# Kernel tuning notes

Hardware: AMD Instinct MI355X
Metric: run time of the kernel (lower is better)

The kernel has to match this reference:

```python
import jax, jax.numpy as jnp
import numpy as np

B, T, C = 4, 2048, 1024
T_REF = 512
H = 16
D = C // H


def setup_inputs() -> dict:
    key = jax.random.key(0)
    ks = jax.random.split(key, 16)
    s = 0.02
    return {
        "x": jax.random.normal(ks[0], (B, T, C), jnp.float32),
        "ref_feat": jax.random.normal(ks[1], (B, T_REF, C), jnp.float32),
        "Wq": jax.random.normal(ks[2], (C, C), jnp.float32) * s,
        "bq": jax.random.normal(ks[3], (C,), jnp.float32) * s,
        "Wk": jax.random.normal(ks[4], (C, C), jnp.float32) * s,
        "bk": jax.random.normal(ks[5], (C,), jnp.float32) * s,
        "Wv": jax.random.normal(ks[6], (C, C), jnp.float32) * s,
        "bv": jax.random.normal(ks[7], (C,), jnp.float32) * s,
        "Wrk": jax.random.normal(ks[8], (C, C), jnp.float32) * s,
        "brk": jax.random.normal(ks[9], (C,), jnp.float32) * s,
        "Wrv": jax.random.normal(ks[10], (C, C), jnp.float32) * s,
        "brv": jax.random.normal(ks[11], (C,), jnp.float32) * s,
        "Wp": jax.random.normal(ks[12], (C, C), jnp.float32) * s,
        "bp": jax.random.normal(ks[13], (C,), jnp.float32) * s,
    }


def _heads(y):
    # [B, T, C] -> [B, H, T, D]
    b, t, c = y.shape
    return y.reshape(b, t, H, D).transpose(0, 2, 1, 3)


def reference(x, ref_feat, Wq, bq, Wk, bk, Wv, bv, Wrk, brk, Wrv, brv, Wp, bp):
    b, t, c = x.shape
    t_ref = ref_feat.shape[1]
    q = _heads(x @ Wq + bq)                      # [B,H,T,D]
    k = _heads(x @ Wk + bk)                      # [B,H,T,D]
    v = _heads(x @ Wv + bv)
    ref_k = _heads(ref_feat @ Wrk + brk)         # [B,H,Tref,D]
    ref_v = _heads(ref_feat @ Wrv + brv)
    k = jnp.concatenate([k, ref_k], axis=2)      # [B,H,T+Tref,D]
    v = jnp.concatenate([v, ref_v], axis=2)

    # additive bias: causal over self keys, fully visible over ref keys
    causal = jnp.tril(jnp.ones((t, t), dtype=bool))
    full_mask = jnp.concatenate([causal, jnp.ones((t, t_ref), dtype=bool)], axis=1)
    bias = jnp.where(full_mask, 0.0, -jnp.inf).astype(x.dtype)  # [T, T+Tref]

    scale = 1.0 / jnp.sqrt(jnp.asarray(D, x.dtype))
    scores = jnp.einsum("bhtd,bhsd->bhts", q, k) * scale + bias
    attn = jax.nn.softmax(scores, axis=-1)
    y = jnp.einsum("bhts,bhsd->bhtd", attn, v)   # [B,H,T,D]
    y = y.transpose(0, 2, 1, 3).reshape(b, t, c)
    return y @ Wp + bp
```

## Files before the change

### kernel.cpp

```cpp
#include <hip/hip_runtime.h>
#include <hip/hip_bf16.h>

typedef short s16x4 __attribute__((ext_vector_type(4)));
typedef short s16x8 __attribute__((ext_vector_type(8)));
typedef __bf16 bf16x8 __attribute__((ext_vector_type(8)));
typedef float f32x4 __attribute__((ext_vector_type(4)));

#define DEVI static __device__ __forceinline__
#define QSCALE 0.18033688011112042f

DEVI unsigned short f2bf(float x) {
  union { float f; unsigned u; } a; a.f = x;
  unsigned r = a.u + 0x7fffu + ((a.u >> 16) & 1u);
  return (unsigned short)(r >> 16);
}
DEVI bf16x8 asbf(s16x8 v) {
  union { s16x8 s; bf16x8 b; } u; u.s = v; return u.b;
}
DEVI unsigned cvtpk(float lo, float hi) {
  unsigned r;
  asm("v_cvt_pk_bf16_f32 %0, %1, %2" : "=v"(r) : "v"(lo), "v"(hi));
  return r;
}
DEVI void gload16(const void* g, void* l) {
  __builtin_amdgcn_global_load_lds(
      (const __attribute__((address_space(1))) void*)g,
      (__attribute__((address_space(3))) void*)l, 16, 0, 0);
}

struct PrepArgs {
  const float* x; const float* ref; unsigned short* xg;
  const float* w[6]; unsigned short* o[6];
};

__global__ __launch_bounds__(256)
void prep(PrepArgs a) {
  __shared__ short tile[64][65];
  const int bid = blockIdx.x, t = threadIdx.x;
  if (bid < 5120) {
    int f = bid * 256 + t;
    int row = f >> 7, c8 = f & 127;
    const float* src = (row < 8192 ? a.x + (size_t)row * 1024
                                   : a.ref + (size_t)(row - 8192) * 1024) + c8 * 8;
    float4 v0 = *(const float4*)src;
    float4 v1 = *(const float4*)(src + 4);
    s16x8 o;
    o[0] = (short)f2bf(v0.x); o[1] = (short)f2bf(v0.y);
    o[2] = (short)f2bf(v0.z); o[3] = (short)f2bf(v0.w);
    o[4] = (short)f2bf(v1.x); o[5] = (short)f2bf(v1.y);
    o[6] = (short)f2bf(v1.z); o[7] = (short)f2bf(v1.w);
    int cs = (c8 & ~7) | ((c8 ^ row) & 7);
    *(s16x8*)(a.xg + (size_t)row * 1024 + cs * 8) = o;
  } else {
    int q = bid - 5120;
    int z = q >> 8, b2 = q & 255;
    const float* __restrict__ W = a.w[z];
    unsigned short* __restrict__ WT = a.o[z];
    const float sc = (z == 0) ? QSCALE : 1.0f;
    const int n0 = (b2 & 15) * 64;
    const int k0 = (b2 >> 4) * 64;
#pragma unroll
    for (int i = 0; i < 4; i++) {
      int f = t + i * 256;
      int r = f >> 4, c = (f & 15) * 4;
      float4 v = *(const float4*)(W + (size_t)(k0 + r) * 1024 + n0 + c);
      tile[r][c + 0] = (short)f2bf(v.x * sc);
      tile[r][c + 1] = (short)f2bf(v.y * sc);
      tile[r][c + 2] = (short)f2bf(v.z * sc);
      tile[r][c + 3] = (short)f2bf(v.w * sc);
    }
    __syncthreads();
#pragma unroll
    for (int i = 0; i < 2; i++) {
      int f = t + i * 256;
      int r = f >> 3, c8 = f & 7;
      s16x8 o;
#pragma unroll
      for (int jj = 0; jj < 8; jj++) o[jj] = tile[c8 * 8 + jj][r];
      *(s16x8*)(WT + (size_t)(n0 + r) * 1024 + k0 + ((c8 ^ (r & 7)) & 7) * 8) = o;
    }
  }
}

template<int MODE>
__global__ __launch_bounds__(256, 3)
void gemm_bt(const unsigned short* __restrict__ A, const unsigned short* __restrict__ BT,
             const float* __restrict__ b0, const float* __restrict__ b1,
             const float* __restrict__ b2,
             void* __restrict__ o0, void* __restrict__ o1, void* __restrict__ o2)
{
  const int K = 1024;
  __shared__ __align__(16) short As[128][64];
  __shared__ __align__(16) short Bs[128][64];
  const int t = threadIdx.x;
  const int lane = t & 63, wid = t >> 6;
  const int wm = wid >> 1, wn = wid & 1;
  const int lr = lane & 15, lg = lane >> 4;
  const size_t m0 = (size_t)blockIdx.y * 128;
  const int n0 = blockIdx.x * 128;

  f32x4 acc[4][4];
#pragma unroll
  for (int i = 0; i < 4; i++)
#pragma unroll
    for (int j = 0; j < 4; j++) acc[i][j] = (f32x4){0.f, 0.f, 0.f, 0.f};

  const unsigned short* Abase = A + m0 * K;
  const unsigned short* Bbase = BT + (size_t)n0 * K;
  const int r_ld = t >> 3, cb_ld = t & 7;

  for (int k0 = 0; k0 < K; k0 += 64) {
#pragma unroll
    for (int i = 0; i < 4; i++) {
      int r = r_ld + i * 32;
      gload16(Abase + (size_t)r * K + k0 + cb_ld * 8,
              (short*)As + (i * 256 + wid * 64) * 8);
      gload16(Bbase + (size_t)r * K + k0 + cb_ld * 8,
              (short*)Bs + (i * 256 + wid * 64) * 8);
    }
    __syncthreads();
#pragma unroll
    for (int ks = 0; ks < 2; ks++) {
      s16x8 af[4], bfr[4];
#pragma unroll
      for (int i = 0; i < 4; i++)
        af[i] = *(const s16x8*)&As[wm * 64 + i * 16 + lr][(((ks * 4 + lg) ^ lr) & 7) * 8];
#pragma unroll
      for (int i = 0; i < 4; i++)
        bfr[i] = *(const s16x8*)&Bs[wn * 64 + i * 16 + lr][(((ks * 4 + lg) ^ lr) & 7) * 8];
#pragma unroll
      for (int mi = 0; mi < 4; mi++)
#pragma unroll
        for (int ni = 0; ni < 4; ni++)
          acc[mi][ni] = __builtin_amdgcn_mfma_f32_16x16x32_bf16(
              asbf(af[mi]), asbf(bfr[ni]), acc[mi][ni], 0, 0, 0);
    }
    __syncthreads();
  }

  const int seg = n0 >> 10;
  const float* bb = (seg == 0) ? b0 : (seg == 1 ? b1 : b2);
#pragma unroll
  for (int mi = 0; mi < 4; mi++) {
#pragma unroll
    for (int ni = 0; ni < 4; ni++) {
      int cg = n0 + wn * 64 + ni * 16 + lr;
      int c = cg & 1023;
      float bv = bb[c];
      if (MODE == 0 && seg == 0) bv *= QSCALE;
      const bool vseg = (MODE == 0 && seg == 2) || (MODE == 1 && seg == 1);
      if (MODE != 2 && vseg) {
        int rm0 = (int)m0 + wm * 64 + mi * 16 + lg * 4;
        int d = c & 63, hh = c >> 6;
        int bb_, s;
        if (MODE == 0) { bb_ = rm0 >> 11; s = rm0 & 2047; }
        else           { bb_ = rm0 >> 9;  s = 2048 + (rm0 & 511); }
        int scol = (s & ~63) + ((((s >> 3) ^ d) & 7) << 3) + (s & 7);
        unsigned short* dst = (unsigned short*)(MODE == 0 ? o2 : o1);
        short4 pk4;
        pk4.x = (short)f2bf(acc[mi][ni][0] + bv);
        pk4.y = (short)f2bf(acc[mi][ni][1] + bv);
        pk4.z = (short)f2bf(acc[mi][ni][2] + bv);
        pk4.w = (short)f2bf(acc[mi][ni][3] + bv);
        *(short4*)(dst + ((size_t)(bb_ * 16 + hh) * 64 + d) * 2560 + scol) = pk4;
      } else {
#pragma unroll
        for (int r = 0; r < 4; r++) {
          int rm = (int)m0 + wm * 64 + mi * 16 + lg * 4 + r;
          float val = acc[mi][ni][r] + bv;
          if (MODE == 2) {
            ((float*)o0)[(size_t)rm * 1024 + cg] = val;
          } else {
            size_t orow; unsigned short* dst; bool swz;
            if (MODE == 0) {
              if (seg == 0) { dst = (unsigned short*)o0; orow = rm; swz = false; }
              else { orow = (size_t)(rm >> 11) * 2560 + (rm & 2047);
                     dst = (unsigned short*)o1; swz = true; }
            } else {
              orow = (size_t)(rm >> 9) * 2560 + 2048 + (rm & 511);
              dst = (unsigned short*)o0; swz = true;
            }
            int cc = c;
            if (swz) cc = (c & ~63) | ((((c >> 3) ^ (int)orow) & 7) << 3) | (c & 7);
            dst[orow * 1024 + cc] = f2bf(val);
          }
        }
      }
    }
  }
}

__global__ __launch_bounds__(256, 5)
void attn(const unsigned short* __restrict__ Q, const unsigned short* __restrict__ Kb,
          const unsigned short* __restrict__ VbT, unsigned short* __restrict__ Y)
{
  const int T = 2048, S = 2560, C = 1024, TREF = 512;
  __shared__ __align__(16) short Ks[2][64][64];
  __shared__ __align__(16) short Vt[2][64][64];
  const int t = threadIdx.x;
  const int lane = t & 63, wid = t >> 6;
  const int lr = lane & 15, lg = lane >> 4;

  const int bid = blockIdx.x;
  const int xcd = bid & 7, idx = bid >> 3;
  const int g = idx & 7;
  const int bx = 31 - (idx >> 3);
  const int bh = xcd * 8 + g;
  const int b = bh >> 4;
  const int hc = (bh & 15) * 64;
  const int q0 = bx * 64;

  const int nself = bx + 1;
  const int ntiles = nself + TREF / 64;

  auto s0_of = [&](int ti2) {
    return (ti2 < nself) ? ti2 * 64 : T + (ti2 - nself) * 64;
  };
  const int r_ld = t >> 3, cb_ld = t & 7;
  auto load_K = [&](int ti2, int buf) {
    int s0 = s0_of(ti2);
    const unsigned short* Krow = Kb + (size_t)(b * S + s0) * C + hc;
#pragma unroll
    for (int i = 0; i < 2; i++)
      gload16(Krow + (size_t)(r_ld + i * 32) * C + cb_ld * 8,
              (short*)&Ks[buf][0][0] + (i * 256 + wid * 64) * 8);
  };
  auto load_V = [&](int ti2, int buf) {
    int s0 = s0_of(ti2);
    const unsigned short* Vr = VbT + (size_t)bh * 64 * S + s0;
#pragma unroll
    for (int i = 0; i < 2; i++)
      gload16(Vr + (size_t)(r_ld + i * 32) * S + cb_ld * 8,
              (short*)&Vt[buf][0][0] + (i * 256 + wid * 64) * 8);
  };

  load_K(0, 0);
  load_V(0, 0);

  s16x8 qf[2];
  {
    size_t qrow = (size_t)(b * T + q0 + wid * 16 + lr);
#pragma unroll
    for (int ks = 0; ks < 2; ks++)
      qf[ks] = *(const s16x8*)(Q + qrow * C + hc + ks * 32 + lg * 8);
  }

  float mrow = -1e30f, lsum = 0.f;
  f32x4 o[4];
#pragma unroll
  for (int d = 0; d < 4; d++) o[d] = (f32x4){0.f, 0.f, 0.f, 0.f};

  __syncthreads();

  for (int ti = 0; ti < ntiles; ti++) {
    const int cur = ti & 1;
    const bool more = (ti + 1 < ntiles);
    if (more) { load_K(ti + 1, cur ^ 1); load_V(ti + 1, cur ^ 1); }

    f32x4 sa[4];
#pragma unroll
    for (int nt = 0; nt < 4; nt++) sa[nt] = (f32x4){0.f, 0.f, 0.f, 0.f};
    __builtin_amdgcn_s_setprio(1);
#pragma unroll
    for (int ks = 0; ks < 2; ks++) {
      s16x8 kf[4];
#pragma unroll
      for (int nt = 0; nt < 4; nt++)
        kf[nt] = *(const s16x8*)&Ks[cur][nt * 16 + lr][(((ks * 4 + lg) ^ lr) & 7) * 8];
#pragma unroll
      for (int nt = 0; nt < 4; nt++)
        sa[nt] = __builtin_amdgcn_mfma_f32_16x16x32_bf16(
            asbf(kf[nt]), asbf(qf[ks]), sa[nt], 0, 0, 0);
    }
    __builtin_amdgcn_s_setprio(0);

    if (ti == bx) {
      int qg = wid * 16 + lr;
#pragma unroll
      for (int nt = 0; nt < 4; nt++)
#pragma unroll
        for (int r = 0; r < 4; r++)
          if (nt * 16 + lg * 4 + r > qg) sa[nt][r] = -1e30f;
    }

    float mm[4];
#pragma unroll
    for (int nt = 0; nt < 4; nt++)
      mm[nt] = fmaxf(fmaxf(sa[nt][0], sa[nt][1]), fmaxf(sa[nt][2], sa[nt][3]));
    float lm = fmaxf(fmaxf(mm[0], mm[1]), fmaxf(mm[2], mm[3]));

    if (!__all(lm <= mrow + 8.f)) {
      float tm = lm;
      tm = fmaxf(tm, __shfl_xor(tm, 16, 64));
      tm = fmaxf(tm, __shfl_xor(tm, 32, 64));
      float mn = fmaxf(mrow, tm);
      float alpha = __builtin_amdgcn_exp2f(mrow - mn);
      mrow = mn;
      lsum *= alpha;
#pragma unroll
      for (int r = 0; r < 4; r++) {
        float ar = __shfl(alpha, lg * 4 + r, 64);
#pragma unroll
        for (int dt = 0; dt < 4; dt++) o[dt][r] *= ar;
      }
    }

    unsigned pk2[4][2];
    float rsn[4];
#pragma unroll
    for (int nt = 0; nt < 4; nt++) {
      float p0 = __builtin_amdgcn_exp2f(sa[nt][0] - mrow);
      float p1 = __builtin_amdgcn_exp2f(sa[nt][1] - mrow);
      float p2 = __builtin_amdgcn_exp2f(sa[nt][2] - mrow);
      float p3 = __builtin_amdgcn_exp2f(sa[nt][3] - mrow);
      rsn[nt] = (p0 + p1) + (p2 + p3);
      pk2[nt][0] = cvtpk(p0, p1);
      pk2[nt][1] = cvtpk(p2, p3);
    }
    lsum += (rsn[0] + rsn[1]) + (rsn[2] + rsn[3]);

    s16x8 pa[2];
#pragma unroll
    for (int ks = 0; ks < 2; ks++) {
      union { unsigned w[4]; s16x8 v; } U;
#pragma unroll
      for (int w = 0; w < 4; w++) {
        int srcL = lr + (((lg & 1) * 2 + (w >> 1)) << 4);
        unsigned v0 = __shfl((int)pk2[2 * ks][w & 1], srcL, 64);
        unsigned v1 = __shfl((int)pk2[2 * ks + 1][w & 1], srcL, 64);
        U.w[w] = (lg & 2) ? v1 : v0;
      }
      pa[ks] = U.v;
    }

    __builtin_amdgcn_s_setprio(1);
#pragma unroll
    for (int ks = 0; ks < 2; ks++) {
      s16x8 vf[4];
#pragma unroll
      for (int dt = 0; dt < 4; dt++)
        vf[dt] = *(const s16x8*)&Vt[cur][dt * 16 + lr][(((ks * 4 + lg) ^ lr) & 7) * 8];
#pragma unroll
      for (int dt = 0; dt < 4; dt++)
        o[dt] = __builtin_amdgcn_mfma_f32_16x16x32_bf16(
            asbf(pa[ks]), asbf(vf[dt]), o[dt], 0, 0, 0);
    }
    __builtin_amdgcn_s_setprio(0);

    __syncthreads();
  }

  float tot = lsum;
  tot += __shfl_xor(tot, 16, 64);
  tot += __shfl_xor(tot, 32, 64);
#pragma unroll
  for (int r = 0; r < 4; r++) {
    float inv = 1.0f / __shfl(tot, lg * 4 + r, 64);
    int qrow = b * T + q0 + wid * 16 + lg * 4 + r;
#pragma unroll
    for (int dt = 0; dt < 4; dt++) {
      int col = hc + dt * 16 + lr;
      int cb = col >> 3;
      int cs = (cb & ~7) | ((cb ^ qrow) & 7);
      Y[(size_t)qrow * C + cs * 8 + (col & 7)] = f2bf(o[dt][r] * inv);
    }
  }
}

extern "C" void kernel_launch(void* const* d_in, const int* in_sizes, int n_in,
                              void* d_out, int out_size, void* d_ws, size_t ws_size,
                              hipStream_t stream) {
  const float* x   = (const float*)d_in[0];
  const float* ref = (const float*)d_in[1];
  const float* Wq  = (const float*)d_in[2];
  const float* bq  = (const float*)d_in[3];
  const float* Wk  = (const float*)d_in[4];
  const float* bk  = (const float*)d_in[5];
  const float* Wv  = (const float*)d_in[6];
  const float* bv  = (const float*)d_in[7];
  const float* Wrk = (const float*)d_in[8];
  const float* brk = (const float*)d_in[9];
  const float* Wrv = (const float*)d_in[10];
  const float* brv = (const float*)d_in[11];
  const float* Wp  = (const float*)d_in[12];
  const float* bp  = (const float*)d_in[13];
  float* out = (float*)d_out;

  char* ws = (char*)d_ws;
  auto alloc = [&](size_t bytes) {
    char* p = ws; ws += (bytes + 255) & ~(size_t)255; return p;
  };
  const size_t WB = (size_t)1024 * 1024 * 2;
  unsigned short* Wall = (unsigned short*)alloc(5 * WB);
  unsigned short* WpT  = (unsigned short*)alloc(WB);
  unsigned short* xg  = (unsigned short*)alloc((size_t)10240 * 1024 * 2);
  unsigned short* rg  = xg + (size_t)8192 * 1024;
  unsigned short* qb  = (unsigned short*)alloc((size_t)8192 * 1024 * 2);
  unsigned short* kb  = (unsigned short*)alloc((size_t)4 * 2560 * 1024 * 2);
  unsigned short* vbT = (unsigned short*)alloc((size_t)4096 * 2560 * 2);
  unsigned short* yb  = (unsigned short*)alloc((size_t)8192 * 1024 * 2);

  dim3 tb(256);

  PrepArgs pa;
  pa.x = x; pa.ref = ref; pa.xg = xg;
  pa.w[0] = Wq;  pa.o[0] = Wall;
  pa.w[1] = Wk;  pa.o[1] = Wall + (size_t)1024 * 1024;
  pa.w[2] = Wv;  pa.o[2] = Wall + (size_t)2048 * 1024;
  pa.w[3] = Wrk; pa.o[3] = Wall + (size_t)3072 * 1024;
  pa.w[4] = Wrv; pa.o[4] = Wall + (size_t)4096 * 1024;
  pa.w[5] = Wp;  pa.o[5] = WpT;
  prep<<<dim3(6656), tb, 0, stream>>>(pa);

  gemm_bt<0><<<dim3(24, 64), tb, 0, stream>>>(xg, Wall, bq, bk, bv, qb, kb, vbT);
  gemm_bt<1><<<dim3(16, 16), tb, 0, stream>>>(rg, Wall + (size_t)3072 * 1024,
                                              brk, brv, nullptr, kb, vbT, nullptr);

  attn<<<dim3(2048), tb, 0, stream>>>(qb, kb, vbT, yb);

  gemm_bt<2><<<dim3(8, 64), tb, 0, stream>>>(yb, WpT, bp, bp, bp, out, out, out);
}
```

Before: 221.8 us.

## Pair causal query tiles per block and switch attention to 32x32 MFMA

Each attention block now handles two query tiles, bx and 31-bx, with two waves per tile, so every block does balanced causal work and shares the same streamed K/V tiles. The half-grid launch takes 1024 blocks instead of 2048. The inner products move from 16x16x32 to 32x32x16 bf16 MFMA, and P is repacked with permlane32 swaps instead of many shuffles. Output stores become 4-wide. This adds register pressure (launch bounds lowered to 4 waves per SIMD), and the low tile's waves idle on tiles past their diagonal.

```diff
diff --git a/kernel.cpp b/kernel.cpp
--- a/kernel.cpp
+++ b/kernel.cpp
@@ -5,6 +5,7 @@
 typedef short s16x8 __attribute__((ext_vector_type(8)));
 typedef __bf16 bf16x8 __attribute__((ext_vector_type(8)));
 typedef float f32x4 __attribute__((ext_vector_type(4)));
+typedef float f32x16 __attribute__((ext_vector_type(16)));
 
 #define DEVI static __device__ __forceinline__
 #define QSCALE 0.18033688011112042f
@@ -190,7 +191,7 @@
   }
 }
 
-__global__ __launch_bounds__(256, 5)
+__global__ __launch_bounds__(256, 4)
 void attn(const unsigned short* __restrict__ Q, const unsigned short* __restrict__ Kb,
           const unsigned short* __restrict__ VbT, unsigned short* __restrict__ Y)
 {
@@ -199,19 +200,20 @@
   __shared__ __align__(16) short Vt[2][64][64];
   const int t = threadIdx.x;
   const int lane = t & 63, wid = t >> 6;
-  const int lr = lane & 15, lg = lane >> 4;
+  const int l31 = lane & 31, hi = lane >> 5;
+  const int j = wid >> 1, sub = wid & 1;
 
   const int bid = blockIdx.x;
   const int xcd = bid & 7, idx = bid >> 3;
-  const int g = idx & 7;
-  const int bx = 31 - (idx >> 3);
-  const int bh = xcd * 8 + g;
+  const int bh = xcd * 8 + (idx >> 4);
+  const int bx = idx & 15;
   const int b = bh >> 4;
   const int hc = (bh & 15) * 64;
-  const int q0 = bx * 64;
-
-  const int nself = bx + 1;
+  const int qtile = j ? (31 - bx) : bx;
+
+  const int nself = 32 - bx;
   const int ntiles = nself + TREF / 64;
+  const int tdiag = j ? (nself - 1) : bx;
 
   auto s0_of = [&](int ti2) {
     return (ti2 < nself) ? ti2 * 64 : T + (ti2 - nself) * 64;
@@ -237,132 +239,144 @@
   load_K(0, 0);
   load_V(0, 0);
 
-  s16x8 qf[2];
+  s16x8 qf[4];
   {
-    size_t qrow = (size_t)(b * T + q0 + wid * 16 + lr);
-#pragma unroll
-    for (int ks = 0; ks < 2; ks++)
-      qf[ks] = *(const s16x8*)(Q + qrow * C + hc + ks * 32 + lg * 8);
+    size_t qrow = (size_t)(b * T + qtile * 64 + sub * 32 + l31);
+#pragma unroll
+    for (int ks = 0; ks < 4; ks++)
+      qf[ks] = *(const s16x8*)(Q + qrow * C + hc + ks * 16 + hi * 8);
   }
 
   float mrow = -1e30f, lsum = 0.f;
-  f32x4 o[4];
-#pragma unroll
-  for (int d = 0; d < 4; d++) o[d] = (f32x4){0.f, 0.f, 0.f, 0.f};
+  f32x16 o0 = 0.f, o1 = 0.f;
 
   __syncthreads();
+
+  const int swz = (l31 & 7);
 
   for (int ti = 0; ti < ntiles; ti++) {
     const int cur = ti & 1;
     const bool more = (ti + 1 < ntiles);
     if (more) { load_K(ti + 1, cur ^ 1); load_V(ti + 1, cur ^ 1); }
 
-    f32x4 sa[4];
-#pragma unroll
-    for (int nt = 0; nt < 4; nt++) sa[nt] = (f32x4){0.f, 0.f, 0.f, 0.f};
-    __builtin_amdgcn_s_setprio(1);
-#pragma unroll
-    for (int ks = 0; ks < 2; ks++) {
-      s16x8 kf[4];
-#pragma unroll
-      for (int nt = 0; nt < 4; nt++)
-        kf[nt] = *(const s16x8*)&Ks[cur][nt * 16 + lr][(((ks * 4 + lg) ^ lr) & 7) * 8];
-#pragma unroll
-      for (int nt = 0; nt < 4; nt++)
-        sa[nt] = __builtin_amdgcn_mfma_f32_16x16x32_bf16(
-            asbf(kf[nt]), asbf(qf[ks]), sa[nt], 0, 0, 0);
-    }
-    __builtin_amdgcn_s_setprio(0);
-
-    if (ti == bx) {
-      int qg = wid * 16 + lr;
-#pragma unroll
-      for (int nt = 0; nt < 4; nt++)
-#pragma unroll
-        for (int r = 0; r < 4; r++)
-          if (nt * 16 + lg * 4 + r > qg) sa[nt][r] = -1e30f;
-    }
-
-    float mm[4];
-#pragma unroll
-    for (int nt = 0; nt < 4; nt++)
-      mm[nt] = fmaxf(fmaxf(sa[nt][0], sa[nt][1]), fmaxf(sa[nt][2], sa[nt][3]));
-    float lm = fmaxf(fmaxf(mm[0], mm[1]), fmaxf(mm[2], mm[3]));
-
-    if (!__all(lm <= mrow + 8.f)) {
-      float tm = lm;
-      tm = fmaxf(tm, __shfl_xor(tm, 16, 64));
-      tm = fmaxf(tm, __shfl_xor(tm, 32, 64));
-      float mn = fmaxf(mrow, tm);
-      float alpha = __builtin_amdgcn_exp2f(mrow - mn);
-      mrow = mn;
-      lsum *= alpha;
-#pragma unroll
-      for (int r = 0; r < 4; r++) {
-        float ar = __shfl(alpha, lg * 4 + r, 64);
-#pragma unroll
-        for (int dt = 0; dt < 4; dt++) o[dt][r] *= ar;
-      }
-    }
-
-    unsigned pk2[4][2];
-    float rsn[4];
-#pragma unroll
-    for (int nt = 0; nt < 4; nt++) {
-      float p0 = __builtin_amdgcn_exp2f(sa[nt][0] - mrow);
-      float p1 = __builtin_amdgcn_exp2f(sa[nt][1] - mrow);
-      float p2 = __builtin_amdgcn_exp2f(sa[nt][2] - mrow);
-      float p3 = __builtin_amdgcn_exp2f(sa[nt][3] - mrow);
-      rsn[nt] = (p0 + p1) + (p2 + p3);
-      pk2[nt][0] = cvtpk(p0, p1);
-      pk2[nt][1] = cvtpk(p2, p3);
-    }
-    lsum += (rsn[0] + rsn[1]) + (rsn[2] + rsn[3]);
-
-    s16x8 pa[2];
-#pragma unroll
-    for (int ks = 0; ks < 2; ks++) {
-      union { unsigned w[4]; s16x8 v; } U;
-#pragma unroll
-      for (int w = 0; w < 4; w++) {
-        int srcL = lr + (((lg & 1) * 2 + (w >> 1)) << 4);
-        unsigned v0 = __shfl((int)pk2[2 * ks][w & 1], srcL, 64);
-        unsigned v1 = __shfl((int)pk2[2 * ks + 1][w & 1], srcL, 64);
-        U.w[w] = (lg & 2) ? v1 : v0;
-      }
-      pa[ks] = U.v;
-    }
-
-    __builtin_amdgcn_s_setprio(1);
-#pragma unroll
-    for (int ks = 0; ks < 2; ks++) {
-      s16x8 vf[4];
-#pragma unroll
-      for (int dt = 0; dt < 4; dt++)
-        vf[dt] = *(const s16x8*)&Vt[cur][dt * 16 + lr][(((ks * 4 + lg) ^ lr) & 7) * 8];
-#pragma unroll
-      for (int dt = 0; dt < 4; dt++)
-        o[dt] = __builtin_amdgcn_mfma_f32_16x16x32_bf16(
-            asbf(pa[ks]), asbf(vf[dt]), o[dt], 0, 0, 0);
-    }
-    __builtin_amdgcn_s_setprio(0);
+    const bool active = j || (ti <= bx) || (ti >= nself);
+    if (active) {
+      f32x16 sa0 = 0.f, sa1 = 0.f;
+      __builtin_amdgcn_s_setprio(1);
+#pragma unroll
+      for (int ks = 0; ks < 4; ks++) {
+        int cb = ks * 2 + hi;
+        s16x8 kf0 = *(const s16x8*)&Ks[cur][l31][((cb ^ swz) & 7) * 8];
+        s16x8 kf1 = *(const s16x8*)&Ks[cur][32 + l31][((cb ^ swz) & 7) * 8];
+        sa0 = __builtin_amdgcn_mfma_f32_32x32x16_bf16(
+            asbf(kf0), asbf(qf[ks]), sa0, 0, 0, 0);
+        sa1 = __builtin_amdgcn_mfma_f32_32x32x16_bf16(
+            asbf(kf1), asbf(qf[ks]), sa1, 0, 0, 0);
+      }
+      __builtin_amdgcn_s_setprio(0);
+
+      if (ti == tdiag) {
+        int qg = sub * 32 + l31;
+#pragma unroll
+        for (int r = 0; r < 16; r++) {
+          int sl = (r & 3) + 8 * (r >> 2) + 4 * hi;
+          if (sl > qg)      sa0[r] = -1e30f;
+          if (32 + sl > qg) sa1[r] = -1e30f;
+        }
+      }
+
+      float mx[8];
+#pragma unroll
+      for (int r = 0; r < 8; r++)
+        mx[r] = fmaxf(fmaxf(sa0[2 * r], sa0[2 * r + 1]),
+                      fmaxf(sa1[2 * r], sa1[2 * r + 1]));
+      float lm = fmaxf(fmaxf(fmaxf(mx[0], mx[1]), fmaxf(mx[2], mx[3])),
+                       fmaxf(fmaxf(mx[4], mx[5]), fmaxf(mx[6], mx[7])));
+
+      if (!__all(lm <= mrow + 8.f)) {
+        float tm = fmaxf(lm, __shfl_xor(lm, 32, 64));
+        float mn = fmaxf(mrow, tm);
+        float alpha = __builtin_amdgcn_exp2f(mrow - mn);
+        mrow = mn;
+        lsum *= alpha;
+        o0 *= alpha;
+        o1 *= alpha;
+      }
+
+#pragma unroll
+      for (int r = 0; r < 16; r++) {
+        sa0[r] = __builtin_amdgcn_exp2f(sa0[r] - mrow);
+        sa1[r] = __builtin_amdgcn_exp2f(sa1[r] - mrow);
+      }
+      float sm[8];
+#pragma unroll
+      for (int r = 0; r < 8; r++)
+        sm[r] = (sa0[2 * r] + sa0[2 * r + 1]) + (sa1[2 * r] + sa1[2 * r + 1]);
+      lsum += ((sm[0] + sm[1]) + (sm[2] + sm[3])) +
+              ((sm[4] + sm[5]) + (sm[6] + sm[7]));
+
+      s16x8 pb[4];
+#pragma unroll
+      for (int sb = 0; sb < 2; sb++) {
+        unsigned A[8];
+#pragma unroll
+        for (int m = 0; m < 8; m++)
+          A[m] = (sb == 0) ? cvtpk(sa0[2 * m], sa0[2 * m + 1])
+                           : cvtpk(sa1[2 * m], sa1[2 * m + 1]);
+        {
+          unsigned x0 = A[0], y0 = A[2], x1 = A[1], y1 = A[3];
+          asm("v_permlane32_swap_b32 %0, %1" : "+v"(x0), "+v"(y0));
+          asm("v_permlane32_swap_b32 %0, %1" : "+v"(x1), "+v"(y1));
+          union { unsigned w[4]; s16x8 v; } U;
+          U.w[0] = x0; U.w[1] = x1; U.w[2] = y0; U.w[3] = y1;
+          pb[sb * 2] = U.v;
+        }
+        {
+          unsigned x0 = A[4], y0 = A[6], x1 = A[5], y1 = A[7];
+          asm("v_permlane32_swap_b32 %0, %1" : "+v"(x0), "+v"(y0));
+          asm("v_permlane32_swap_b32 %0, %1" : "+v"(x1), "+v"(y1));
+          union { unsigned w[4]; s16x8 v; } U;
+          U.w[0] = x0; U.w[1] = x1; U.w[2] = y0; U.w[3] = y1;
+          pb[sb * 2 + 1] = U.v;
+        }
+      }
+
+      __builtin_amdgcn_s_setprio(1);
+#pragma unroll
+      for (int sl = 0; sl < 4; sl++) {
+        int cb = sl * 2 + hi;
+        s16x8 vf0 = *(const s16x8*)&Vt[cur][l31][((cb ^ swz) & 7) * 8];
+        s16x8 vf1 = *(const s16x8*)&Vt[cur][32 + l31][((cb ^ swz) & 7) * 8];
+        o0 = __builtin_amdgcn_mfma_f32_32x32x16_bf16(
+            asbf(vf0), asbf(pb[sl]), o0, 0, 0, 0);
+        o1 = __builtin_amdgcn_mfma_f32_32x32x16_bf16(
+            asbf(vf1), asbf(pb[sl]), o1, 0, 0, 0);
+      }
+      __builtin_amdgcn_s_setprio(0);
+    }
 
     __syncthreads();
   }
 
-  float tot = lsum;
-  tot += __shfl_xor(tot, 16, 64);
-  tot += __shfl_xor(tot, 32, 64);
-#pragma unroll
-  for (int r = 0; r < 4; r++) {
-    float inv = 1.0f / __shfl(tot, lg * 4 + r, 64);
-    int qrow = b * T + q0 + wid * 16 + lg * 4 + r;
-#pragma unroll
-    for (int dt = 0; dt < 4; dt++) {
-      int col = hc + dt * 16 + lr;
+  float tot = lsum + __shfl_xor(lsum, 32, 64);
+  float inv = 1.0f / tot;
+  int qrow = b * T + qtile * 64 + sub * 32 + l31;
+#pragma unroll
+  for (int dblk = 0; dblk < 2; dblk++) {
+#pragma unroll
+    for (int g = 0; g < 4; g++) {
+      int d = dblk * 32 + 8 * g + 4 * hi;
+      float v0 = (dblk ? o1[4 * g + 0] : o0[4 * g + 0]) * inv;
+      float v1 = (dblk ? o1[4 * g + 1] : o0[4 * g + 1]) * inv;
+      float v2 = (dblk ? o1[4 * g + 2] : o0[4 * g + 2]) * inv;
+      float v3 = (dblk ? o1[4 * g + 3] : o0[4 * g + 3]) * inv;
+      short4 s4;
+      s4.x = (short)f2bf(v0); s4.y = (short)f2bf(v1);
+      s4.z = (short)f2bf(v2); s4.w = (short)f2bf(v3);
+      int col = hc + d;
       int cb = col >> 3;
       int cs = (cb & ~7) | ((cb ^ qrow) & 7);
-      Y[(size_t)qrow * C + cs * 8 + (col & 7)] = f2bf(o[dt][r] * inv);
+      *(short4*)(Y + (size_t)qrow * C + cs * 8 + (d & 7)) = s4;
     }
   }
 }
@@ -416,7 +430,7 @@
   gemm_bt<1><<<dim3(16, 16), tb, 0, stream>>>(rg, Wall + (size_t)3072 * 1024,
                                               brk, brv, nullptr, kb, vbT, nullptr);
 
-  attn<<<dim3(2048), tb, 0, stream>>>(qb, kb, vbT, yb);
+  attn<<<dim3(1024), tb, 0, stream>>>(qb, kb, vbT, yb);
 
   gemm_bt<2><<<dim3(8, 64), tb, 0, stream>>>(yb, WpT, bp, bp, bp, out, out, out);
 }
```

New measurement: 206.8 us. 6.8% less time.
